# Kernel optimization log

Measured on AMD Instinct MI355X. Metric: run time of the kernel, lower is better.

## Reference

```python
import jax, jax.numpy as jnp
import numpy as np

D_MODEL = 1024
NUM_HEADS = 16
HEAD_DIM = D_MODEL // NUM_HEADS
B, S = 4, 2048


def setup_inputs() -> dict:
    key = jax.random.key(0)
    ks = jax.random.split(key, 11)
    scale = 1.0 / np.sqrt(D_MODEL)
    inp = {
        "query": jax.random.normal(ks[0], (B, S, D_MODEL), dtype=jnp.float32),
        "key": jax.random.normal(ks[1], (B, S, D_MODEL), dtype=jnp.float32),
        "value": jax.random.normal(ks[2], (B, S, D_MODEL), dtype=jnp.float32),
        "Wq": jax.random.normal(ks[3], (D_MODEL, D_MODEL), dtype=jnp.float32) * scale,
        "bq": jnp.zeros((D_MODEL,), dtype=jnp.float32),
        "Wk": jax.random.normal(ks[4], (D_MODEL, D_MODEL), dtype=jnp.float32) * scale,
        "bk": jnp.zeros((D_MODEL,), dtype=jnp.float32),
        "Wv": jax.random.normal(ks[5], (D_MODEL, D_MODEL), dtype=jnp.float32) * scale,
        "bv": jnp.zeros((D_MODEL,), dtype=jnp.float32),
        "Wo": jax.random.normal(ks[6], (D_MODEL, D_MODEL), dtype=jnp.float32) * scale,
        "bo": jnpp.zeros((D_MODEL,), dtype=jnp.float32) if False else jnp.zeros((D_MODEL,), dtype=jnp.float32),
    }
    return inp


def reference(query, key, value, Wq, bq, Wk, bk, Wv, bv, Wo, bo):
    # Linear projections (torch Linear: x @ W.T + b), split into heads: [B,H,S,Dh]
    def split_heads(x):
        b, s, _ = x.shape
        return x.reshape(b, s, NUM_HEADS, HEAD_DIM).transpose(0, 2, 1, 3)

    q = split_heads(query @ Wq.T + bq)
    k = split_heads(key @ Wk.T + bk)
    v = split_heads(value @ Wv.T + bv)

    # Explicit attention: [B,H,S,S] scores, softmax, AV
    scores = jnp.einsum("bhqd,bhkd->bhqk", q, k) / np.sqrt(HEAD_DIM).astype(np.float32)
    attn = jax.nn.softmax(scores, axis=-1)
    ctx = jnp.einsum("bhqk,bhkd->bhqd", attn, v)

    # Merge heads and output projection
    b = ctx.shape[0]
    ctx = ctx.transpose(0, 2, 1, 3).reshape(b, -1, D_MODEL)
    return ctx @ Wo.T + bo
```

## Files before the change

kernel.cpp:

```cpp
#include <hip/hip_runtime.h>
#include <stdint.h>

#define DMODEL 1024
#define NHEADS 16
#define HDIM   64
#define BB     4
#define SS     2048
#define MM     (BB*SS)
#define QKV_ELEMS ((size_t)8388608)

typedef unsigned short ushort_t;
typedef __bf16    bf16x8  __attribute__((ext_vector_type(8)));
typedef _Float16  half4   __attribute__((ext_vector_type(4)));
typedef _Float16  half2_t __attribute__((ext_vector_type(2)));
typedef float     floatx4 __attribute__((ext_vector_type(4)));

__device__ inline ushort_t f32_to_bf16(float f) {
    union { float f; uint32_t u; } v; v.f = f;
    uint32_t r = v.u + 0x7FFF + ((v.u >> 16) & 1);
    return (ushort_t)(r >> 16);
}
__device__ inline ushort_t f32_to_f16u(float f) {
    union { _Float16 h; ushort_t u; } v; v.h = (_Float16)f; return v.u;
}
__device__ inline half2_t pkrtz(float a, float b) {
    return __builtin_bit_cast(half2_t, __builtin_amdgcn_cvt_pkrtz(a, b));
}
__device__ inline void glds16(const void* g, void* l) {
    __builtin_amdgcn_global_load_lds(
        (const __attribute__((address_space(1))) unsigned int*)g,
        (__attribute__((address_space(3))) unsigned int*)l, 16, 0, 0);
}

__global__ __launch_bounds__(256) void convert_bf16(const float* __restrict__ in,
                                                    ushort_t* __restrict__ out) {
    size_t i = ((size_t)blockIdx.x * 256 + threadIdx.x) * 8;
    float4 a = *(const float4*)&in[i];
    float4 b = *(const float4*)&in[i + 4];
    ushort_t t[8];
    t[0] = f32_to_bf16(a.x); t[1] = f32_to_bf16(a.y);
    t[2] = f32_to_bf16(a.z); t[3] = f32_to_bf16(a.w);
    t[4] = f32_to_bf16(b.x); t[5] = f32_to_bf16(b.y);
    t[6] = f32_to_bf16(b.z); t[7] = f32_to_bf16(b.w);
    *(uint4*)&out[i] = *(uint4*)t;
}

__global__ __launch_bounds__(256) void convert_w3(
    const float* __restrict__ w0, const float* __restrict__ w1, const float* __restrict__ w2,
    ushort_t* __restrict__ o0, ushort_t* __restrict__ o1, ushort_t* __restrict__ o2) {
    const float* src = (blockIdx.y == 0) ? w0 : (blockIdx.y == 1) ? w1 : w2;
    ushort_t*    dst = (blockIdx.y == 0) ? o0 : (blockIdx.y == 1) ? o1 : o2;
    size_t i = ((size_t)blockIdx.x * 256 + threadIdx.x) * 8;
    float4 a = *(const float4*)&src[i];
    float4 b = *(const float4*)&src[i + 4];
    ushort_t t[8];
    t[0] = f32_to_bf16(a.x); t[1] = f32_to_bf16(a.y);
    t[2] = f32_to_bf16(a.z); t[3] = f32_to_bf16(a.w);
    t[4] = f32_to_bf16(b.x); t[5] = f32_to_bf16(b.y);
    t[6] = f32_to_bf16(b.z); t[7] = f32_to_bf16(b.w);
    *(uint4*)&dst[i] = *(uint4*)t;
}

template<int OUT>
__global__ __launch_bounds__(256) void gemm_bf16(
    const ushort_t* __restrict__ A, const ushort_t* __restrict__ W,
    const float* __restrict__ bias, void* __restrict__ O, float scale)
{
    __shared__ ushort_t As[2 * 128 * 32];
    __shared__ ushort_t Bs[2 * 128 * 32];

    const int tid  = threadIdx.x;
    const int lane = tid & 63;
    const int quad = lane >> 4;
    const int l15  = lane & 15;
    const int wid  = tid >> 6;
    const int wr   = wid >> 1, wc = wid & 1;
    const int m0   = blockIdx.y * 128;
    const int n0   = blockIdx.x * 128;

    floatx4 acc[4][4];
    #pragma unroll
    for (int i = 0; i < 4; i++)
        #pragma unroll
        for (int j = 0; j < 4; j++)
            acc[i][j] = (floatx4){0.f, 0.f, 0.f, 0.f};

    #pragma unroll
    for (int j = 0; j < 2; j++) {
        const int p  = tid + j * 256;
        const int ph = p << 4;
        const int lg = ph ^ (((ph >> 7) & 7) << 4);
        const int row = lg >> 6, cc = (lg >> 4) & 3;
        glds16(&A[(size_t)(m0 + row) * DMODEL + cc * 8], (char*)As + ph);
        glds16(&W[(size_t)(n0 + row) * DMODEL + cc * 8], (char*)Bs + ph);
    }

    for (int k0 = 0; k0 < DMODEL; k0 += 32) {
        const int cbB = ((k0 >> 5) & 1) * 8192;
        const int nbB = 8192 - cbB;
        __syncthreads();
        const int kn = (k0 + 32) & (DMODEL - 1);
        #pragma unroll
        for (int j = 0; j < 2; j++) {
            const int p  = tid + j * 256;
            const int ph = p << 4;
            const int lg = ph ^ (((ph >> 7) & 7) << 4);
            const int row = lg >> 6, cc = (lg >> 4) & 3;
            glds16(&A[(size_t)(m0 + row) * DMODEL + kn + cc * 8], (char*)As + nbB + ph);
            glds16(&W[(size_t)(n0 + row) * DMODEL + kn + cc * 8], (char*)Bs + nbB + ph);
        }
        bf16x8 af[4], bfv[4];
        #pragma unroll
        for (int i = 0; i < 4; i++) {
            const int r = wr * 64 + i * 16 + l15;
            const int L = (r << 6) | (quad << 4);
            af[i] = *(const bf16x8*)((const char*)As + cbB + (L ^ (((r >> 1) & 7) << 4)));
        }
        #pragma unroll
        for (int j = 0; j < 4; j++) {
            const int r = wc * 64 + j * 16 + l15;
            const int L = (r << 6) | (quad << 4);
            bfv[j] = *(const bf16x8*)((const char*)Bs + cbB + (L ^ (((r >> 1) & 7) << 4)));
        }
        #pragma unroll
        for (int i = 0; i < 4; i++)
            #pragma unroll
            for (int j = 0; j < 4; j++)
                acc[i][j] = __builtin_amdgcn_mfma_f32_16x16x32_bf16(af[i], bfv[j], acc[i][j], 0, 0, 0);
    }

    #pragma unroll
    for (int j = 0; j < 4; j++) {
        const int n = n0 + wc * 64 + j * 16 + l15;
        const float bn = bias[n];
        #pragma unroll
        for (int i = 0; i < 4; i++) {
            #pragma unroll
            for (int r = 0; r < 4; r++) {
                const int m = m0 + wr * 64 + i * 16 + quad * 4 + r;
                float v = (acc[i][j][r] + bn) * scale;
                if (OUT == 0) {
                    const int b = m >> 11, s = m & 2047;
                    const int hh = n >> 6, dh = n & 63;
                    ((ushort_t*)O)[(((size_t)(b * NHEADS + hh)) * SS + s) * HDIM + dh] = f32_to_bf16(v);
                } else if (OUT == 1) {
                    const int b = m >> 11, s = m & 2047;
                    const int hh = n >> 6, dh = n & 63;
                    ((ushort_t*)O)[(((size_t)(b * NHEADS + hh)) * SS + s) * HDIM + dh] = f32_to_f16u(v);
                } else {
                    ((float*)O)[(size_t)m * DMODEL + n] = v;
                }
            }
        }
    }
}

__global__ __launch_bounds__(256, 4) void attn_kernel(
    const ushort_t* __restrict__ Q, const ushort_t* __restrict__ K,
    const ushort_t* __restrict__ V, ushort_t* __restrict__ ctx)
{
    constexpr int LDV = 72;
    constexpr int VOFF = 2 * 4096;
    __shared__ ushort_t smem[2 * 4096 + 2 * 64 * LDV];
    ushort_t* Tr = smem;

    const int tid  = threadIdx.x;
    const int lane = tid & 63;
    const int wid  = tid >> 6;
    const int quad = lane >> 4;
    const int l15  = lane & 15;
    const int bid  = blockIdx.x;
    const int bh   = (bid & 7) * 8 + (bid >> 7);
    const int b    = bh >> 4, h = bh & 15;
    const int q0   = ((bid >> 3) & 15) * 128 + wid * 32;

    const ushort_t* Qb = Q + (size_t)bh * SS * HDIM;
    const ushort_t* Kb = K + (size_t)bh * SS * HDIM;
    const ushort_t* Vb = V + (size_t)bh * SS * HDIM;

    bf16x8 qf[2][2];
    #pragma unroll
    for (int qt = 0; qt < 2; qt++)
        #pragma unroll
        for (int c = 0; c < 2; c++)
            qf[qt][c] = *(const bf16x8*)&Qb[(size_t)(q0 + qt * 16 + l15) * HDIM + c * 32 + quad * 8];

    floatx4 acc[2][4];
    #pragma unroll
    for (int qt = 0; qt < 2; qt++)
        #pragma unroll
        for (int dt = 0; dt < 4; dt++)
            acc[qt][dt] = (floatx4){0.f, 0.f, 0.f, 0.f};
    float mrun[2] = {-1e30f, -1e30f};
    float lrun[2] = {0.f, 0.f};

    const int kp = tid & 31;
    const int dc = tid >> 5;

    #pragma unroll
    for (int j = 0; j < 2; j++) {
        const int p = tid + j * 256, row = p >> 3, cc = (p & 7) ^ (row & 7);
        glds16(&Kb[(size_t)row * HDIM + cc * 8], &smem[p * 8]);
    }
    {
        ushort_t ua[8], ub[8];
        *(uint4*)ua = *(const uint4*)&Vb[(size_t)(2 * kp) * HDIM + dc * 8];
        *(uint4*)ub = *(const uint4*)&Vb[(size_t)(2 * kp + 1) * HDIM + dc * 8];
        #pragma unroll
        for (int i = 0; i < 8; i++)
            *(uint32_t*)&smem[VOFF + (dc * 8 + i) * LDV + 2 * kp] = (uint32_t)ua[i] | ((uint32_t)ub[i] << 16);
    }

    const half2_t one2 = {(_Float16)1.f, (_Float16)1.f};

    for (int kt = 0; kt < SS; kt += 64) {
        const int cur = ((kt >> 6) & 1);
        const int ko  = cur * 4096;
        const int kon = 4096 - ko;
        const int vo  = VOFF + cur * (64 * LDV);
        const int von = VOFF + (64 * LDV) - cur * (64 * LDV);
        __syncthreads();

        const int ktn = (kt + 64) & (SS - 1);
        #pragma unroll
        for (int j = 0; j < 2; j++) {
            const int p = tid + j * 256, row = p >> 3, cc = (p & 7) ^ (row & 7);
            glds16(&Kb[(size_t)(ktn + row) * HDIM + cc * 8], &smem[kon + p * 8]);
        }
        ushort_t ua[8], ub[8];
        *(uint4*)ua = *(const uint4*)&Vb[(size_t)(ktn + 2 * kp) * HDIM + dc * 8];
        *(uint4*)ub = *(const uint4*)&Vb[(size_t)(ktn + 2 * kp + 1) * HDIM + dc * 8];

        bf16x8 kf[4][2];
        #pragma unroll
        for (int nt = 0; nt < 4; nt++) {
            const int row = nt * 16 + l15;
            #pragma unroll
            for (int c = 0; c < 2; c++) {
                const int pos = (c * 4 + quad) ^ (row & 7);
                kf[nt][c] = *(const bf16x8*)&smem[ko + row * 64 + pos * 8];
            }
        }
        half4 vf[4][4];
        #pragma unroll
        for (int kb = 0; kb < 4; kb++)
            #pragma unroll
            for (int dt = 0; dt < 4; dt++)
                vf[kb][dt] = *(const half4*)&smem[vo + (dt * 16 + l15) * LDV + kb * 16 + quad * 4];

        #pragma unroll
        for (int qt = 0; qt < 2; qt++) {
            floatx4 s[4];
            #pragma unroll
            for (int nt = 0; nt < 4; nt++) {
                floatx4 cz = (floatx4){0.f, 0.f, 0.f, 0.f};
                cz = __builtin_amdgcn_mfma_f32_16x16x32_bf16(kf[nt][0], qf[qt][0], cz, 0, 0, 0);
                cz = __builtin_amdgcn_mfma_f32_16x16x32_bf16(kf[nt][1], qf[qt][1], cz, 0, 0, 0);
                s[nt] = cz;
            }
            float mx = s[0][0];
            #pragma unroll
            for (int nt = 0; nt < 4; nt++)
                #pragma unroll
                for (int r = 0; r < 4; r++) mx = fmaxf(mx, s[nt][r]);
            mx = fmaxf(mx, __shfl_xor(mx, 16));
            mx = fmaxf(mx, __shfl_xor(mx, 32));
            const float mnew  = fmaxf(mrun[qt], mx);
            const float alpha = __builtin_amdgcn_exp2f(mrun[qt] - mnew);
            mrun[qt] = mnew;

            float ps = 0.f;
            half4 pf[4];
            #pragma unroll
            for (int nt = 0; nt < 4; nt++) {
                const float p0 = __builtin_amdgcn_exp2f(s[nt][0] - mnew);
                const float p1 = __builtin_amdgcn_exp2f(s[nt][1] - mnew);
                const float p2 = __builtin_amdgcn_exp2f(s[nt][2] - mnew);
                const float p3 = __builtin_amdgcn_exp2f(s[nt][3] - mnew);
                const half2_t ha = pkrtz(p0, p1);
                const half2_t hb = pkrtz(p2, p3);
                ps = __builtin_amdgcn_fdot2(ha, one2, ps, false);
                ps = __builtin_amdgcn_fdot2(hb, one2, ps, false);
                union { half4 h4; half2_t h2[2]; } u;
                u.h2[0] = ha; u.h2[1] = hb;
                pf[nt] = u.h4;
            }
            ps += __shfl_xor(ps, 16);
            ps += __shfl_xor(ps, 32);
            lrun[qt] = lrun[qt] * alpha + ps;

            #pragma unroll
            for (int dt = 0; dt < 4; dt++) acc[qt][dt] *= alpha;
            #pragma unroll
            for (int kb = 0; kb < 4; kb++)
                #pragma unroll
                for (int dt = 0; dt < 4; dt++)
                    acc[qt][dt] = __builtin_amdgcn_mfma_f32_16x16x16f16(vf[kb][dt], pf[kb], acc[qt][dt], 0, 0, 0);
        }

        #pragma unroll
        for (int i = 0; i < 8; i++)
            *(uint32_t*)&smem[von + (dc * 8 + i) * LDV + 2 * kp] = (uint32_t)ua[i] | ((uint32_t)ub[i] << 16);
    }

    __syncthreads();
    const float inv0 = 1.f / lrun[0], inv1 = 1.f / lrun[1];
    ushort_t* Tw = Tr + wid * (32 * LDV);
    #pragma unroll
    for (int qt = 0; qt < 2; qt++) {
        const float inv = qt ? inv1 : inv0;
        #pragma unroll
        for (int dt = 0; dt < 4; dt++)
            #pragma unroll
            for (int r = 0; r < 4; r++)
                Tw[(qt * 16 + l15) * LDV + dt * 16 + quad * 4 + r] = f32_to_bf16(acc[qt][dt][r] * inv);
    }
    const int row = lane >> 1, hf = lane & 1;
    const ushort_t* src = Tw + row * LDV + hf * 32;
    ushort_t* dst = ctx + ((size_t)(b * SS) + q0 + row) * DMODEL + h * HDIM + hf * 32;
    #pragma unroll
    for (int i = 0; i < 4; i++)
        *(uint4*)(dst + i * 8) = *(const uint4*)(src + i * 8);
}

extern "C" void kernel_launch(void* const* d_in, const int* in_sizes, int n_in,
                              void* d_out, int out_size, void* d_ws, size_t ws_size,
                              hipStream_t stream) {
    (void)in_sizes; (void)n_in; (void)out_size; (void)ws_size;
    const float* query = (const float*)d_in[0];
    const float* key_  = (const float*)d_in[1];
    const float* value = (const float*)d_in[2];
    const float* Wq = (const float*)d_in[3];
    const float* bq = (const float*)d_in[4];
    const float* Wk = (const float*)d_in[5];
    const float* bk = (const float*)d_in[6];
    const float* Wv = (const float*)d_in[7];
    const float* bv = (const float*)d_in[8];
    const float* Wo = (const float*)d_in[9];
    const float* bo = (const float*)d_in[10];
    float* out = (float*)d_out;

    ushort_t* tmp = (ushort_t*)d_ws;
    ushort_t* Qw  = tmp + QKV_ELEMS;
    ushort_t* Kw  = Qw + QKV_ELEMS;
    ushort_t* Vw  = Kw + QKV_ELEMS;
    ushort_t* ctx = tmp;
    ushort_t* Wqb = (ushort_t*)d_out;
    ushort_t* Wkb = Wqb + 1048576;
    ushort_t* Wvb = Wkb + 1048576;
    ushort_t* Wob = Qw;

    dim3 blk(256);
    dim3 gg(DMODEL / 128, MM / 128);

    hipLaunchKernelGGL(convert_w3, dim3(512, 3), blk, 0, stream, Wq, Wk, Wv, Wqb, Wkb, Wvb);

    hipLaunchKernelGGL(convert_bf16, dim3(4096), blk, 0, stream, query, tmp);
    hipLaunchKernelGGL((gemm_bf16<0>), gg, blk, 0, stream, tmp, Wqb, bq, (void*)Qw, 0.18033688011f);
    hipLaunchKernelGGL(convert_bf16, dim3(4096), blk, 0, stream, key_, tmp);
    hipLaunchKernelGGL((gemm_bf16<0>), gg, blk, 0, stream, tmp, Wkb, bk, (void*)Kw, 1.0f);
    hipLaunchKernelGGL(convert_bf16, dim3(4096), blk, 0, stream, value, tmp);
    hipLaunchKernelGGL((gemm_bf16<1>), gg, blk, 0, stream, tmp, Wvb, bv, (void*)Vw, 1.0f);

    hipLaunchKernelGGL(attn_kernel, dim3(1024), blk, 0, stream, Qw, Kw, Vw, ctx);

    hipLaunchKernelGGL(convert_bf16, dim3(512), blk, 0, stream, Wo, Wob);
    hipLaunchKernelGGL((gemm_bf16<2>), gg, blk, 0, stream, ctx, Wob, bo, (void*)out, 1.0f);
}
```

Measured before the change: 399.6 us.

## Triple-buffer GEMM shared-memory tiles with explicit vmcnt waits

Switches the bf16 projection GEMM from double to triple buffering of its A/W tiles in LDS. Loads are now issued two K-steps ahead, and the code waits with s_waitcnt vmcnt(4) instead of an implicit full wait, so more global-to-LDS loads can be in flight while MFMAs run. The cost is 50% more LDS per block, which may lower occupancy, plus hand-written waitcnt and barrier logic that is correct only if no other vector-memory operations are outstanding.

```diff
diff --git a/kernel.cpp b/kernel.cpp
--- a/kernel.cpp
+++ b/kernel.cpp
@@ -66,8 +66,8 @@
     const ushort_t* __restrict__ A, const ushort_t* __restrict__ W,
     const float* __restrict__ bias, void* __restrict__ O, float scale)
 {
-    __shared__ ushort_t As[2 * 128 * 32];
-    __shared__ ushort_t Bs[2 * 128 * 32];
+    __shared__ ushort_t As[3 * 4096];
+    __shared__ ushort_t Bs[3 * 4096];
 
     const int tid  = threadIdx.x;
     const int lane = tid & 63;
@@ -85,29 +85,31 @@
         for (int j = 0; j < 4; j++)
             acc[i][j] = (floatx4){0.f, 0.f, 0.f, 0.f};
 
-    #pragma unroll
-    for (int j = 0; j < 2; j++) {
-        const int p  = tid + j * 256;
-        const int ph = p << 4;
-        const int lg = ph ^ (((ph >> 7) & 7) << 4);
-        const int row = lg >> 6, cc = (lg >> 4) & 3;
-        glds16(&A[(size_t)(m0 + row) * DMODEL + cc * 8], (char*)As + ph);
-        glds16(&W[(size_t)(n0 + row) * DMODEL + cc * 8], (char*)Bs + ph);
-    }
-
-    for (int k0 = 0; k0 < DMODEL; k0 += 32) {
-        const int cbB = ((k0 >> 5) & 1) * 8192;
-        const int nbB = 8192 - cbB;
-        __syncthreads();
-        const int kn = (k0 + 32) & (DMODEL - 1);
+    auto stage = [&](int kk, int bufB) {
         #pragma unroll
         for (int j = 0; j < 2; j++) {
             const int p  = tid + j * 256;
             const int ph = p << 4;
             const int lg = ph ^ (((ph >> 7) & 7) << 4);
             const int row = lg >> 6, cc = (lg >> 4) & 3;
-            glds16(&A[(size_t)(m0 + row) * DMODEL + kn + cc * 8], (char*)As + nbB + ph);
-            glds16(&W[(size_t)(n0 + row) * DMODEL + kn + cc * 8], (char*)Bs + nbB + ph);
+            glds16(&A[(size_t)(m0 + row) * DMODEL + kk + cc * 8], (char*)As + bufB + ph);
+            glds16(&W[(size_t)(n0 + row) * DMODEL + kk + cc * 8], (char*)Bs + bufB + ph);
+        }
+    };
+
+    stage(0, 0);
+    stage(32, 8192);
+
+    int cbB = 0;
+    for (int k0 = 0; k0 < DMODEL; k0 += 32) {
+        if (k0 + 32 < DMODEL) asm volatile("s_waitcnt vmcnt(4)" ::: "memory");
+        else                  asm volatile("s_waitcnt vmcnt(0)" ::: "memory");
+        __builtin_amdgcn_s_barrier();
+        __builtin_amdgcn_sched_barrier(0);
+        const int k2 = k0 + 64;
+        if (k2 < DMODEL) {
+            int nbB = cbB + 16384; if (nbB >= 24576) nbB -= 24576;
+            stage(k2, nbB);
         }
         bf16x8 af[4], bfv[4];
         #pragma unroll
@@ -127,6 +129,7 @@
             #pragma unroll
             for (int j = 0; j < 4; j++)
                 acc[i][j] = __builtin_amdgcn_mfma_f32_16x16x32_bf16(af[i], bfv[j], acc[i][j], 0, 0, 0);
+        cbB += 8192; if (cbB == 24576) cbB = 0;
     }
 
     #pragma unroll
```

New measurement: 393.7 us. No clear change (-1.5%).
